# Kernel tuning notes

Hardware: AMD Instinct MI355X
Metric: run time of the kernel (lower is better)

The kernel has to match this reference:

```python
import jax, jax.numpy as jnp
import numpy as np
from jax.ops import segment_sum

N_NODES = 100000
N_EDGES = 1600000

def setup_inputs() -> dict:
    key = jax.random.key(0)
    ks = jax.random.split(key, 16)
    s = 0.1
    return {
        "x": jax.random.normal(ks[0], (N_NODES, 8), jnp.float32),
        "edge_index": jax.random.randint(ks[1], (2, N_EDGES), 0, N_NODES, jnp.int32),
        "W1l": jax.random.normal(ks[2], (8, 128)) * s,
        "W1r": jax.random.normal(ks[3], (8, 128)) * s,
        "b1": jnp.zeros((128,)),
        "W2l": jax.random.normal(ks[4], (128, 128)) * s,
        "W2r": jax.random.normal(ks[5], (128, 128)) * s,
        "b2": jnp.zeros((128,)),
        "W3l": jax.random.normal(ks[6], (128, 1)) * s,
        "W3r": jax.random.normal(ks[7], (128, 1)) * s,
        "b3": jnp.zeros((1,)),
        "Ta1_W": jax.random.normal(ks[8], (4, 8, 8)) * s,
        "Ta1_b": jnp.zeros((8,)),
        "Ta2_W": jax.random.normal(ks[9], (4, 8, 1)) * s,
        "Ta2_b": jnp.zeros((1,)),
        "Tb1_W": jax.random.normal(ks[10], (10, 8, 8)) * s,
        "Tb1_b": jnp.zeros((8,)),
        "Tb2_W": jax.random.normal(ks[11], (10, 8, 1)) * s,
        "Tb2_b": jnp.zeros((1,)),
        "lin2_W": jax.random.normal(ks[12], (2, 1)) * s,
        "lin2_b": jnp.zeros((1,)),
        "lin1_W": jax.random.normal(ks[13], (2, 1)) * s,
        "lin1_b": jnp.zeros((1,)),
    }

def reference(x, edge_index, W1l, W1r, b1, W2l, W2r, b2, W3l, W3r, b3,
              Ta1_W, Ta1_b, Ta2_W, Ta2_b, Tb1_W, Tb1_b, Tb2_W, Tb2_b,
              lin2_W, lin2_b, lin1_W, lin1_b):
    N = x.shape[0]
    src, dst = edge_index[0], edge_index[1]  # message flows src -> dst

    # in-degree of each target node (edge weight = 1)
    deg = segment_sum(jnp.ones_like(src, dtype=x.dtype), dst, num_segments=N)

    # --- SAGEConv: lin_l(mean_{j in N(i)} x_j) + lin_r(x_i) + bias ---
    inv_deg = jnp.where(deg > 0, 1.0 / jnp.maximum(deg, 1.0), 0.0)
    def sage(h, Wl, Wr, b):
        agg = segment_sum(h[src], dst, num_segments=N) * inv_deg[:, None]
        return agg @ Wl + h @ Wr + b

    # --- TAGConv: sym-normalized adjacency powers, no self loops ---
    dinv = jnp.where(deg > 0, jax.lax.rsqrt(jnp.maximum(deg, 1.0)), 0.0)
    norm = dinv[src] * dinv[dst]  # [E]
    def tag(h, Ws, b):  # Ws: [K+1, in, out]
        out = h @ Ws[0]
        for k in range(1, Ws.shape[0]):
            h = segment_sum(h[src] * norm[:, None], dst, num_segments=N)
            out = out + h @ Ws[k]
        return out + b

    relu = jax.nn.relu
    x1 = relu(sage(x, W1l, W1r, b1))
    x1 = relu(sage(x1, W2l, W2r, b2))
    x1 = relu(sage(x1, W3l, W3r, b3))

    x2 = relu(tag(x, Ta1_W, Ta1_b))
    x2 = relu(tag(x2, Ta2_W, Ta2_b))

    x3 = relu(tag(x, Tb1_W, Tb1_b))
    x3 = relu(tag(x3, Tb2_W, Tb2_b))

    x23 = relu(jnp.concatenate([x2, x3], axis=1) @ lin2_W + lin2_b)
    out = relu(jnp.concatenate([x1, x23], axis=1) @ lin1_W + lin1_b)
    return out
```

## Files before the change

### kernel.cpp

```cpp
#include <hip/hip_runtime.h>

#define NN 100000
#define NE 1600000
#define TPB 256

__global__ void k_init(int* __restrict__ deg, int* __restrict__ cursor, int* __restrict__ counter) {
    int i = blockIdx.x * TPB + threadIdx.x;
    if (i < NN) { deg[i] = 0; cursor[i] = 0; }
    if (i == 0) counter[0] = 0;
}

__global__ void k_deg(const int* __restrict__ dst, int* __restrict__ deg) {
    int e = blockIdx.x * TPB + threadIdx.x;
    if (e < NE) atomicAdd(&deg[dst[e]], 1);
}

__global__ void k_prep(const int* __restrict__ deg, float* __restrict__ inv_deg,
                       float* __restrict__ dinv, int* __restrict__ row_start,
                       int* __restrict__ counter) {
    int i = blockIdx.x * TPB + threadIdx.x;
    int lane = threadIdx.x & 63;
    int d = (i < NN) ? deg[i] : 0;
    int incl = d;
    #pragma unroll
    for (int o = 1; o < 64; o <<= 1) {
        int v = __shfl_up(incl, o, 64);
        if (lane >= o) incl += v;
    }
    int total = __shfl(incl, 63, 64);
    int base = 0;
    if (lane == 63) base = atomicAdd(counter, total);
    base = __shfl(base, 63, 64);
    if (i < NN) {
        row_start[i] = base + incl - d;
        inv_deg[i] = d > 0 ? 1.0f / (float)d : 0.0f;
        dinv[i]    = d > 0 ? 1.0f / sqrtf((float)d) : 0.0f;
    }
}

__global__ void k_fill(const int* __restrict__ src, const int* __restrict__ dst,
                       const int* __restrict__ row_start, int* __restrict__ cursor,
                       int* __restrict__ col) {
    int e = blockIdx.x * TPB + threadIdx.x;
    if (e < NE) {
        int d = dst[e];
        int p = atomicAdd(&cursor[d], 1);
        col[row_start[d] + p] = src[e];
    }
}

__global__ void k_meanprop8(const float* __restrict__ h, const int* __restrict__ row_start,
                            const int* __restrict__ deg, const float* __restrict__ inv_deg,
                            const int* __restrict__ col, float* __restrict__ out) {
    int t = blockIdx.x * TPB + threadIdx.x;
    if (t >= NN * 2) return;
    int n = t >> 1, half = t & 1;
    int rs = row_start[n], end = rs + deg[n];
    const float4* h4 = (const float4*)h;
    float4 s0 = make_float4(0,0,0,0), s1 = make_float4(0,0,0,0);
    int e = rs + half;
    for (; e + 2 < end; e += 4) {
        int c0 = col[e] * 2, c1 = col[e + 2] * 2;
        float4 a0 = h4[c0], a1 = h4[c0 + 1], b0 = h4[c1], b1 = h4[c1 + 1];
        s0.x += a0.x + b0.x; s0.y += a0.y + b0.y; s0.z += a0.z + b0.z; s0.w += a0.w + b0.w;
        s1.x += a1.x + b1.x; s1.y += a1.y + b1.y; s1.z += a1.z + b1.z; s1.w += a1.w + b1.w;
    }
    if (e < end) {
        int c0 = col[e] * 2;
        float4 a0 = h4[c0], a1 = h4[c0 + 1];
        s0.x += a0.x; s0.y += a0.y; s0.z += a0.z; s0.w += a0.w;
        s1.x += a1.x; s1.y += a1.y; s1.z += a1.z; s1.w += a1.w;
    }
    s0.x += __shfl_xor(s0.x, 1, 64); s0.y += __shfl_xor(s0.y, 1, 64);
    s0.z += __shfl_xor(s0.z, 1, 64); s0.w += __shfl_xor(s0.w, 1, 64);
    s1.x += __shfl_xor(s1.x, 1, 64); s1.y += __shfl_xor(s1.y, 1, 64);
    s1.z += __shfl_xor(s1.z, 1, 64); s1.w += __shfl_xor(s1.w, 1, 64);
    float w = inv_deg[n];
    float4 o = (half == 0) ? s0 : s1;
    o.x *= w; o.y *= w; o.z *= w; o.w *= w;
    ((float4*)out)[n * 2 + half] = o;
}

__global__ __launch_bounds__(1024) void k_meanprop128T(const float* __restrict__ h,
                              const int* __restrict__ row_start,
                              const int* __restrict__ deg, const float* __restrict__ inv_deg,
                              const int* __restrict__ col, float* __restrict__ outT) {
    __shared__ float t[128][33];
    int n0 = blockIdx.x * 32;
    int tid = threadIdx.x;
    int nl = tid >> 5;
    int f4 = tid & 31;
    int n = n0 + nl;
    int rs = row_start[n], end = rs + deg[n];
    const float4* h4 = (const float4*)h;
    float4 s = make_float4(0.f, 0.f, 0.f, 0.f);
    int e = rs;
    for (; e + 3 < end; e += 4) {
        float4 v0 = h4[(size_t)col[e] * 32 + f4];
        float4 v1 = h4[(size_t)col[e + 1] * 32 + f4];
        float4 v2 = h4[(size_t)col[e + 2] * 32 + f4];
        float4 v3 = h4[(size_t)col[e + 3] * 32 + f4];
        s.x += (v0.x + v1.x) + (v2.x + v3.x);
        s.y += (v0.y + v1.y) + (v2.y + v3.y);
        s.z += (v0.z + v1.z) + (v2.z + v3.z);
        s.w += (v0.w + v1.w) + (v2.w + v3.w);
    }
    for (; e < end; ++e) {
        float4 v = h4[(size_t)col[e] * 32 + f4];
        s.x += v.x; s.y += v.y; s.z += v.z; s.w += v.w;
    }
    float w = inv_deg[n];
    t[f4 * 4 + 0][nl] = s.x * w;
    t[f4 * 4 + 1][nl] = s.y * w;
    t[f4 * 4 + 2][nl] = s.z * w;
    t[f4 * 4 + 3][nl] = s.w * w;
    __syncthreads();
    int k = tid >> 3;
    int q = tid & 7;
    float4 v = make_float4(t[k][q * 4], t[k][q * 4 + 1], t[k][q * 4 + 2], t[k][q * 4 + 3]);
    *(float4*)(outT + (size_t)k * NN + n0 + q * 4) = v;
}

__global__ void k_tagstep(const float* __restrict__ q, const int* __restrict__ row_start,
                          const int* __restrict__ deg, const float* __restrict__ dinv,
                          const int* __restrict__ col, float* __restrict__ qout,
                          const float* __restrict__ Wa, const float* __restrict__ Wb,
                          float* __restrict__ outa, float* __restrict__ outb,
                          const float* __restrict__ ba, const float* __restrict__ bb,
                          int fina, int finb) {
    int t = blockIdx.x * TPB + threadIdx.x;
    if (t >= NN * 8) return;
    int n = t >> 3, qd = t & 7;
    int half = qd & 1, epar = qd >> 1;
    int rs = row_start[n], end = rs + deg[n];
    const float4* q4 = (const float4*)q;
    float4 s = make_float4(0,0,0,0);
    int e = rs + epar;
    for (; e + 4 < end; e += 8) {
        int c0 = col[e] * 2 + half, c1 = col[e + 4] * 2 + half;
        float4 a = q4[c0], b = q4[c1];
        s.x += a.x + b.x; s.y += a.y + b.y; s.z += a.z + b.z; s.w += a.w + b.w;
    }
    if (e < end) {
        float4 a = q4[col[e] * 2 + half];
        s.x += a.x; s.y += a.y; s.z += a.z; s.w += a.w;
    }
    #pragma unroll
    for (int o = 2; o < 8; o <<= 1) {
        s.x += __shfl_xor(s.x, o, 64); s.y += __shfl_xor(s.y, o, 64);
        s.z += __shfl_xor(s.z, o, 64); s.w += __shfl_xor(s.w, o, 64);
    }
    float dn = dinv[n];
    float m0 = s.x * dn, m1 = s.y * dn, m2 = s.z * dn, m3 = s.w * dn;
    if (qout && epar == 0) {
        ((float4*)qout)[n * 2 + half] = make_float4(m0 * dn, m1 * dn, m2 * dn, m3 * dn);
    }
    float o0 = __shfl_xor(m0, 1, 64), o1 = __shfl_xor(m1, 1, 64);
    float o2 = __shfl_xor(m2, 1, 64), o3 = __shfl_xor(m3, 1, 64);
    float h[8];
    if (half) {
        h[0] = o0; h[1] = o1; h[2] = o2; h[3] = o3;
        h[4] = m0; h[5] = m1; h[6] = m2; h[7] = m3;
    } else {
        h[0] = m0; h[1] = m1; h[2] = m2; h[3] = m3;
        h[4] = o0; h[5] = o1; h[6] = o2; h[7] = o3;
    }
    int f = qd;
    if (Wa) {
        float v = outa[(size_t)n * 8 + f];
        #pragma unroll
        for (int j = 0; j < 8; ++j) v += h[j] * Wa[j * 8 + f];
        if (fina) v = fmaxf(v + ba[f], 0.f);
        outa[(size_t)n * 8 + f] = v;
    }
    {
        float v = outb[(size_t)n * 8 + f];
        #pragma unroll
        for (int j = 0; j < 8; ++j) v += h[j] * Wb[j * 8 + f];
        if (finb) v = fmaxf(v + bb[f], 0.f);
        outb[(size_t)n * 8 + f] = v;
    }
}

__global__ void k_symprop1n(const float* __restrict__ qin, const float* __restrict__ yk,
                            const int* __restrict__ row_start, const int* __restrict__ deg,
                            const float* __restrict__ dinv, const int* __restrict__ col,
                            float* __restrict__ qout, int qstride) {
    int t = blockIdx.x * TPB + threadIdx.x;
    if (t >= NN * 8) return;
    int n = t >> 3, qd = t & 7;
    int rs = row_start[n], d = deg[n];
    float s = 0.f;
    for (int e = rs + qd; e < rs + d; e += 8) s += qin[col[e]];
    s += __shfl_xor(s, 1, 64);
    s += __shfl_xor(s, 2, 64);
    s += __shfl_xor(s, 4, 64);
    if (qd == 0) {
        float dn = dinv[n];
        qout[(size_t)n * qstride] = dn * (dn * s + yk[n]);
    }
}

__global__ void k_symprop2(const float* __restrict__ q2in, const float* __restrict__ yka,
                           const float* __restrict__ ykb, const int* __restrict__ row_start,
                           const int* __restrict__ deg, const float* __restrict__ dinv,
                           const int* __restrict__ col, float* __restrict__ q2out) {
    int t = blockIdx.x * TPB + threadIdx.x;
    if (t >= NN * 8) return;
    int n = t >> 3, qd = t & 7;
    int rs = row_start[n], d = deg[n];
    const float2* q2 = (const float2*)q2in;
    float sa = 0.f, sb = 0.f;
    for (int e = rs + qd; e < rs + d; e += 8) {
        float2 v = q2[col[e]];
        sa += v.x; sb += v.y;
    }
    sa += __shfl_xor(sa, 1, 64); sa += __shfl_xor(sa, 2, 64); sa += __shfl_xor(sa, 4, 64);
    sb += __shfl_xor(sb, 1, 64); sb += __shfl_xor(sb, 2, 64); sb += __shfl_xor(sb, 4, 64);
    if (qd == 0) {
        float dn = dinv[n];
        ((float2*)q2out)[n] = make_float2(dn * (dn * sa + yka[n]),
                                          dn * (dn * sb + ykb[n]));
    }
}

__global__ void k_symprop2fin(const float* __restrict__ q2in, const float* __restrict__ yka,
                              const float* __restrict__ ykb, const int* __restrict__ row_start,
                              const int* __restrict__ deg, const float* __restrict__ dinv,
                              const int* __restrict__ col,
                              const float* __restrict__ biasa, const float* __restrict__ biasb,
                              const float* __restrict__ x1f,
                              const float* __restrict__ l2w, const float* __restrict__ l2b,
                              const float* __restrict__ l1w, const float* __restrict__ l1b,
                              float* __restrict__ out) {
    int t = blockIdx.x * TPB + threadIdx.x;
    if (t >= NN * 8) return;
    int n = t >> 3, qd = t & 7;
    int rs = row_start[n], d = deg[n];
    const float2* q2 = (const float2*)q2in;
    float sa = 0.f, sb = 0.f;
    for (int e = rs + qd; e < rs + d; e += 8) {
        float2 v = q2[col[e]];
        sa += v.x; sb += v.y;
    }
    sa += __shfl_xor(sa, 1, 64); sa += __shfl_xor(sa, 2, 64); sa += __shfl_xor(sa, 4, 64);
    sb += __shfl_xor(sb, 1, 64); sb += __shfl_xor(sb, 2, 64); sb += __shfl_xor(sb, 4, 64);
    if (qd == 0) {
        float dn = dinv[n];
        float x2 = fmaxf(dn * sa + yka[n] + biasa[0], 0.f);
        float x3 = fmaxf(dn * sb + ykb[n] + biasb[0], 0.f);
        float x23 = fmaxf(x2 * l2w[0] + x3 * l2w[1] + l2b[0], 0.f);
        out[n] = fmaxf(x1f[n] * l1w[0] + x23 * l1w[1] + l1b[0], 0.f);
    }
}

__global__ void k_red8(const float* __restrict__ ylp, const float* __restrict__ yrp,
                       float* __restrict__ yl, float* __restrict__ yr) {
    int n = blockIdx.x * TPB + threadIdx.x;
    if (n >= NN) return;
    float sl = 0.f, sr = 0.f;
    #pragma unroll
    for (int j = 0; j < 8; ++j) {
        sl += ylp[(size_t)j * NN + n];
        sr += yrp[(size_t)j * NN + n];
    }
    yl[n] = sl;
    yr[n] = sr;
}

__global__ void k_sage3(const float* __restrict__ yl, const float* __restrict__ yr,
                        const int* __restrict__ row_start, const int* __restrict__ deg,
                        const float* __restrict__ inv_deg, const int* __restrict__ col,
                        const float* __restrict__ b3, float* __restrict__ x1f) {
    int t = blockIdx.x * TPB + threadIdx.x;
    if (t >= NN * 8) return;
    int n = t >> 3, q = t & 7;
    int rs = row_start[n], d = deg[n];
    float s = 0.f;
    for (int e = rs + q; e < rs + d; e += 8) s += yl[col[e]];
    s += __shfl_xor(s, 1, 64);
    s += __shfl_xor(s, 2, 64);
    s += __shfl_xor(s, 4, 64);
    if (q == 0) x1f[n] = fmaxf(s * inv_deg[n] + yr[n] + b3[0], 0.f);
}

__global__ __launch_bounds__(256) void k_sage1(const float* __restrict__ a8,
                        const float* __restrict__ x,
                        const float* __restrict__ W1l, const float* __restrict__ W1r,
                        const float* __restrict__ b1, float* __restrict__ x1,
                        float* __restrict__ x1T) {
    int n = blockIdx.x * 256 + threadIdx.x;
    int og = blockIdx.y * 8;
    int nc = (n < NN) ? n : (NN - 1);
    float acc[8];
    #pragma unroll
    for (int j = 0; j < 8; ++j) acc[j] = b1[og + j];
    const float* ar = a8 + (size_t)nc * 8;
    const float* xr = x + (size_t)nc * 8;
    #pragma unroll
    for (int k = 0; k < 8; ++k) {
        float av = ar[k], xv = xr[k];
        const float4* wl = (const float4*)(W1l + k * 128 + og);
        const float4* wr = (const float4*)(W1r + k * 128 + og);
        float4 l0 = wl[0], l1 = wl[1], r0 = wr[0], r1 = wr[1];
        acc[0] += av * l0.x + xv * r0.x;
        acc[1] += av * l0.y + xv * r0.y;
        acc[2] += av * l0.z + xv * r0.z;
        acc[3] += av * l0.w + xv * r0.w;
        acc[4] += av * l1.x + xv * r1.x;
        acc[5] += av * l1.y + xv * r1.y;
        acc[6] += av * l1.z + xv * r1.z;
        acc[7] += av * l1.w + xv * r1.w;
    }
    if (n < NN) {
        #pragma unroll
        for (int j = 0; j < 8; ++j) acc[j] = fmaxf(acc[j], 0.f);
        *(float4*)(x1 + (size_t)n * 128 + og)     = make_float4(acc[0], acc[1], acc[2], acc[3]);
        *(float4*)(x1 + (size_t)n * 128 + og + 4) = make_float4(acc[4], acc[5], acc[6], acc[7]);
        #pragma unroll
        for (int j = 0; j < 8; ++j)
            x1T[(size_t)(og + j) * NN + n] = acc[j];
    }
}

__global__ __launch_bounds__(256) void k_sage2f(const float* __restrict__ aT,
        const float* __restrict__ xT, const float* __restrict__ W2l,
        const float* __restrict__ W2r, const float* __restrict__ b2,
        const float* __restrict__ W3l, const float* __restrict__ W3r,
        float* __restrict__ ylp, float* __restrict__ yrp) {
    int xcd = blockIdx.x & 7;
    int s = blockIdx.x >> 3;
    int xblk = xcd * 49 + (s >> 3);
    int ogq = s & 7;
    int og = ogq * 16;
    int n0 = xblk * 256 + threadIdx.x;
    int n = (n0 < NN) ? n0 : (NN - 1);
    float acc[16];
    #pragma unroll
    for (int j = 0; j < 16; ++j) acc[j] = b2[og + j];
    const float* ap = aT + n;
    const float* xp = xT + n;
    const float* wlp = W2l + og;
    const float* wrp = W2r + og;
    #pragma unroll 4
    for (int k = 0; k < 128; ++k) {
        float a = ap[0], xv = xp[0];
        ap += NN; xp += NN;
        const float4* wl4 = (const float4*)(wlp + (k << 7));
        const float4* wr4 = (const float4*)(wrp + (k << 7));
        #pragma unroll
        for (int q = 0; q < 4; ++q) {
            float4 wl = wl4[q], wr = wr4[q];
            acc[q * 4 + 0] += a * wl.x + xv * wr.x;
            acc[q * 4 + 1] += a * wl.y + xv * wr.y;
            acc[q * 4 + 2] += a * wl.z + xv * wr.z;
            acc[q * 4 + 3] += a * wl.w + xv * wr.w;
        }
    }
    float pl = 0.f, pr = 0.f;
    #pragma unroll
    for (int j = 0; j < 16; ++j) {
        float v = fmaxf(acc[j], 0.f);
        pl += v * W3l[og + j];
        pr += v * W3r[og + j];
    }
    if (n0 < NN) {
        ylp[(size_t)ogq * NN + n0] = pl;
        yrp[(size_t)ogq * NN + n0] = pr;
    }
}

__global__ void k_taginit(const float* __restrict__ x, const float* __restrict__ TaW,
                          const float* __restrict__ TbW, const float* __restrict__ dinv,
                          float* __restrict__ outa, float* __restrict__ outb,
                          float* __restrict__ q0) {
    int t = blockIdx.x * TPB + threadIdx.x;
    if (t >= NN * 8) return;
    int n = t >> 3, o = t & 7;
    const float* xr = x + (size_t)n * 8;
    float sa = 0.f, sb = 0.f;
    #pragma unroll
    for (int j = 0; j < 8; ++j) {
        float v = xr[j];
        sa += v * TaW[j * 8 + o];
        sb += v * TbW[j * 8 + o];
    }
    outa[t] = sa;
    outb[t] = sb;
    q0[t] = xr[o] * dinv[n];
}

__global__ void k_tag2projAB(const float* __restrict__ outa, const float* __restrict__ outb,
                             const float* __restrict__ TaW2, const float* __restrict__ TbW2,
                             float* __restrict__ ya, float* __restrict__ yb,
                             const float* __restrict__ dinv,
                             float* __restrict__ q2a, float* __restrict__ qb0) {
    int n = blockIdx.x * TPB + threadIdx.x;
    if (n >= NN) return;
    float dn = dinv[n];
    float ha[8], hb[8];
    #pragma unroll
    for (int j = 0; j < 8; ++j) ha[j] = outa[(size_t)n * 8 + j];
    #pragma unroll
    for (int j = 0; j < 8; ++j) hb[j] = outb[(size_t)n * 8 + j];
    #pragma unroll
    for (int k = 0; k < 4; ++k) {
        float s = 0.f;
        #pragma unroll
        for (int j = 0; j < 8; ++j) s += ha[j] * TaW2[k * 8 + j];
        if (k == 3) q2a[(size_t)n * 2] = s * dn;
        else        ya[(size_t)k * NN + n] = s;
    }
    #pragma unroll
    for (int k = 0; k < 10; ++k) {
        float s = 0.f;
        #pragma unroll
        for (int j = 0; j < 8; ++j) s += hb[j] * TbW2[k * 8 + j];
        if (k == 9) qb0[n] = s * dn;
        else        yb[(size_t)k * NN + n] = s;
    }
}

#define GL(kern, n, ...) \
    kern<<<dim3((unsigned)(((long)(n) + TPB - 1) / TPB)), dim3(TPB), 0, stream>>>(__VA_ARGS__)

extern "C" void kernel_launch(void* const* d_in, const int* in_sizes, int n_in,
                              void* d_out, int out_size, void* d_ws, size_t ws_size,
                              hipStream_t stream) {
    (void)in_sizes; (void)n_in; (void)out_size; (void)ws_size;
    const float* x   = (const float*)d_in[0];
    const int*   ei  = (const int*)d_in[1];
    const int*   src = ei;
    const int*   dst = ei + NE;
    const float* W1l = (const float*)d_in[2];
    const float* W1r = (const float*)d_in[3];
    const float* b1  = (const float*)d_in[4];
    const float* W2l = (const float*)d_in[5];
    const float* W2r = (const float*)d_in[6];
    const float* b2  = (const float*)d_in[7];
    const float* W3l = (const float*)d_in[8];
    const float* W3r = (const float*)d_in[9];
    const float* b3  = (const float*)d_in[10];
    const float* TaW1 = (const float*)d_in[11];
    const float* TaB1 = (const float*)d_in[12];
    const float* TaW2 = (const float*)d_in[13];
    const float* TaB2 = (const float*)d_in[14];
    const float* TbW1 = (const float*)d_in[15];
    const float* TbB1 = (const float*)d_in[16];
    const float* TbW2 = (const float*)d_in[17];
    const float* TbB2 = (const float*)d_in[18];
    const float* l2w = (const float*)d_in[19];
    const float* l2b = (const float*)d_in[20];
    const float* l1w = (const float*)d_in[21];
    const float* l1b = (const float*)d_in[22];
    float* out = (float*)d_out;

    char* p = (char*)d_ws;
    size_t off = 0;
    auto alloc = [&](size_t bytes) -> void* {
        void* r = p + off;
        off = (off + bytes + 255) & ~(size_t)255;
        return r;
    };
    int*   deg       = (int*)  alloc((size_t)NN * 4);
    float* inv_deg   = (float*)alloc((size_t)NN * 4);
    float* dinv      = (float*)alloc((size_t)NN * 4);
    int*   row_start = (int*)  alloc((size_t)NN * 4);
    int*   cursor    = (int*)  alloc((size_t)NN * 4);
    int*   counter   = (int*)  alloc(256);
    int*   col       = (int*)  alloc((size_t)NE * 4);
    float* a8        = (float*)alloc((size_t)NN * 8 * 4);
    float* qA        = (float*)alloc((size_t)NN * 8 * 4);
    float* qB        = (float*)alloc((size_t)NN * 8 * 4);
    float* outa      = (float*)alloc((size_t)NN * 8 * 4);
    float* outb      = (float*)alloc((size_t)NN * 8 * 4);
    float* x1        = (float*)alloc((size_t)NN * 128 * 4);
    float* a128T     = (float*)alloc((size_t)NN * 128 * 4);
    float* x1T       = (float*)alloc((size_t)NN * 128 * 4);
    float* ylp       = (float*)alloc((size_t)NN * 8 * 4);
    float* yrp       = (float*)alloc((size_t)NN * 8 * 4);
    float* yl        = (float*)alloc((size_t)NN * 4);
    float* yr        = (float*)alloc((size_t)NN * 4);
    float* x1f       = (float*)alloc((size_t)NN * 4);
    float* tA        = (float*)alloc((size_t)NN * 4);
    float* tB        = (float*)alloc((size_t)NN * 4);
    float* qb0       = (float*)alloc((size_t)NN * 4);
    float* q2a       = (float*)alloc((size_t)NN * 8);
    float* q2b       = (float*)alloc((size_t)NN * 8);
    float* ya        = (float*)alloc((size_t)NN * 4 * 4);
    float* yb        = (float*)alloc((size_t)NN * 10 * 4);

    GL(k_init, NN, deg, cursor, counter);
    GL(k_deg, NE, dst, deg);
    GL(k_prep, NN, deg, inv_deg, dinv, row_start, counter);
    GL(k_fill, NE, src, dst, row_start, cursor, col);

    GL(k_meanprop8, (long)NN * 2, x, row_start, deg, inv_deg, col, a8);
    k_sage1<<<dim3((NN + 255) / 256, 16), dim3(256), 0, stream>>>(a8, x, W1l, W1r, b1, x1, x1T);
    k_meanprop128T<<<dim3(NN / 32), dim3(1024), 0, stream>>>(x1, row_start, deg, inv_deg, col, a128T);
    k_sage2f<<<dim3(3136), dim3(256), 0, stream>>>(a128T, x1T, W2l, W2r, b2, W3l, W3r, ylp, yrp);
    GL(k_red8, NN, ylp, yrp, yl, yr);
    GL(k_sage3, (long)NN * 8, yl, yr, row_start, deg, inv_deg, col, b3, x1f);

    GL(k_taginit, (long)NN * 8, x, TaW1, TbW1, dinv, outa, outb, qA);
    {
        float* qcur = qA;
        float* qnext = qB;
        for (int k = 1; k <= 9; ++k) {
            float* qout = (k < 9) ? qnext : nullptr;
            const float* Wa = (k <= 3) ? (TaW1 + (size_t)k * 64) : nullptr;
            GL(k_tagstep, (long)NN * 8, qcur, row_start, deg, dinv, col, qout,
               Wa, TbW1 + (size_t)k * 64, outa, outb, TaB1, TbB1,
               (k == 3) ? 1 : 0, (k == 9) ? 1 : 0);
            if (qout) { float* tmp = qcur; qcur = qnext; qnext = tmp; }
        }
    }

    GL(k_tag2projAB, NN, outa, outb, TaW2, TbW2, ya, yb, dinv, q2a, qb0);

    GL(k_symprop1n, (long)NN * 8, qb0, yb + 8 * NN, row_start, deg, dinv, col, tA, 1);
    GL(k_symprop1n, (long)NN * 8, tA,  yb + 7 * NN, row_start, deg, dinv, col, tB, 1);
    GL(k_symprop1n, (long)NN * 8, tB,  yb + 6 * NN, row_start, deg, dinv, col, tA, 1);
    GL(k_symprop1n, (long)NN * 8, tA,  yb + 5 * NN, row_start, deg, dinv, col, tB, 1);
    GL(k_symprop1n, (long)NN * 8, tB,  yb + 4 * NN, row_start, deg, dinv, col, tA, 1);
    GL(k_symprop1n, (long)NN * 8, tA,  yb + 3 * NN, row_start, deg, dinv, col, q2a + 1, 2);

    GL(k_symprop2, (long)NN * 8, q2a, ya + 2 * NN, yb + 2 * NN, row_start, deg, dinv, col, q2b);
    GL(k_symprop2, (long)NN * 8, q2b, ya + 1 * NN, yb + 1 * NN, row_start, deg, dinv, col, q2a);
    GL(k_symprop2fin, (long)NN * 8, q2a, ya + 0 * NN, yb + 0 * NN, row_start, deg, dinv, col,
       TaB2, TbB2, x1f, l2w, l2b, l1w, l1b, out);
}
```

Baseline: 734.9 us.

## Horizontally fuse independent SAGE and TAG branch kernels into combined launches

Turns the separate SAGE, TAG-a and TAG-b kernels into device functions and launches combined kernels whose block ranges dispatch to independent branch work. The TAG-a branch's second-layer propagation is split from the paired float2 propagation and co-scheduled alongside TAG-b steps and SAGE stages. The aim is to fill the GPU better on small, latency-bound graph kernels and cut the launch count. In exchange, block-range dispatch mixes heterogeneous blocks, including 1024-thread blocks shared with tagstep work, which may raise register and LDS pressure and reduce occupancy.

```diff
diff --git a/kernel.cpp b/kernel.cpp
--- a/kernel.cpp
+++ b/kernel.cpp
@@ -3,6 +3,17 @@
 #define NN 100000
 #define NE 1600000
 #define TPB 256
+
+#define NB_MP8    782
+#define NB_TAGI   3125
+#define NB_SAGE1  6272
+#define NB_TAG    3125
+#define NB_MP128T 3125
+#define NB_TAG1K  782
+#define NB_SAGE2F 3136
+#define NB_RED    391
+#define NB_PROP   3125
+#define NB_SAGE3  3125
 
 __global__ void k_init(int* __restrict__ deg, int* __restrict__ cursor, int* __restrict__ counter) {
     int i = blockIdx.x * TPB + threadIdx.x;
@@ -49,10 +60,10 @@
     }
 }
 
-__global__ void k_meanprop8(const float* __restrict__ h, const int* __restrict__ row_start,
-                            const int* __restrict__ deg, const float* __restrict__ inv_deg,
-                            const int* __restrict__ col, float* __restrict__ out) {
-    int t = blockIdx.x * TPB + threadIdx.x;
+__device__ __forceinline__ void dev_meanprop8(int t, const float* __restrict__ h,
+        const int* __restrict__ row_start, const int* __restrict__ deg,
+        const float* __restrict__ inv_deg, const int* __restrict__ col,
+        float* __restrict__ out) {
     if (t >= NN * 2) return;
     int n = t >> 1, half = t & 1;
     int rs = row_start[n], end = rs + deg[n];
@@ -81,13 +92,130 @@
     ((float4*)out)[n * 2 + half] = o;
 }
 
-__global__ __launch_bounds__(1024) void k_meanprop128T(const float* __restrict__ h,
-                              const int* __restrict__ row_start,
-                              const int* __restrict__ deg, const float* __restrict__ inv_deg,
-                              const int* __restrict__ col, float* __restrict__ outT) {
+__device__ __forceinline__ void dev_taginit(int t, const float* __restrict__ x,
+        const float* __restrict__ TaW, const float* __restrict__ TbW,
+        const float* __restrict__ dinv, float* __restrict__ outa,
+        float* __restrict__ outb, float* __restrict__ q0) {
+    if (t >= NN * 8) return;
+    int n = t >> 3, o = t & 7;
+    const float* xr = x + (size_t)n * 8;
+    float sa = 0.f, sb = 0.f;
+    #pragma unroll
+    for (int j = 0; j < 8; ++j) {
+        float v = xr[j];
+        sa += v * TaW[j * 8 + o];
+        sb += v * TbW[j * 8 + o];
+    }
+    outa[t] = sa;
+    outb[t] = sb;
+    q0[t] = xr[o] * dinv[n];
+}
+
+__device__ __forceinline__ void dev_tagstep(int t, const float* __restrict__ q,
+        const int* __restrict__ row_start, const int* __restrict__ deg,
+        const float* __restrict__ dinv, const int* __restrict__ col,
+        float* __restrict__ qout, const float* __restrict__ Wa,
+        const float* __restrict__ Wb, float* __restrict__ outa,
+        float* __restrict__ outb, const float* __restrict__ ba,
+        const float* __restrict__ bb, int fina, int finb) {
+    if (t >= NN * 8) return;
+    int n = t >> 3, qd = t & 7;
+    int half = qd & 1, epar = qd >> 1;
+    int rs = row_start[n], end = rs + deg[n];
+    const float4* q4 = (const float4*)q;
+    float4 s = make_float4(0,0,0,0);
+    int e = rs + epar;
+    for (; e + 4 < end; e += 8) {
+        int c0 = col[e] * 2 + half, c1 = col[e + 4] * 2 + half;
+        float4 a = q4[c0], b = q4[c1];
+        s.x += a.x + b.x; s.y += a.y + b.y; s.z += a.z + b.z; s.w += a.w + b.w;
+    }
+    if (e < end) {
+        float4 a = q4[col[e] * 2 + half];
+        s.x += a.x; s.y += a.y; s.z += a.z; s.w += a.w;
+    }
+    #pragma unroll
+    for (int o = 2; o < 8; o <<= 1) {
+        s.x += __shfl_xor(s.x, o, 64); s.y += __shfl_xor(s.y, o, 64);
+        s.z += __shfl_xor(s.z, o, 64); s.w += __shfl_xor(s.w, o, 64);
+    }
+    float dn = dinv[n];
+    float m0 = s.x * dn, m1 = s.y * dn, m2 = s.z * dn, m3 = s.w * dn;
+    if (qout && epar == 0) {
+        ((float4*)qout)[n * 2 + half] = make_float4(m0 * dn, m1 * dn, m2 * dn, m3 * dn);
+    }
+    float o0 = __shfl_xor(m0, 1, 64), o1 = __shfl_xor(m1, 1, 64);
+    float o2 = __shfl_xor(m2, 1, 64), o3 = __shfl_xor(m3, 1, 64);
+    float h[8];
+    if (half) {
+        h[0] = o0; h[1] = o1; h[2] = o2; h[3] = o3;
+        h[4] = m0; h[5] = m1; h[6] = m2; h[7] = m3;
+    } else {
+        h[0] = m0; h[1] = m1; h[2] = m2; h[3] = m3;
+        h[4] = o0; h[5] = o1; h[6] = o2; h[7] = o3;
+    }
+    int f = qd;
+    if (Wa) {
+        float v = outa[(size_t)n * 8 + f];
+        #pragma unroll
+        for (int j = 0; j < 8; ++j) v += h[j] * Wa[j * 8 + f];
+        if (fina) v = fmaxf(v + ba[f], 0.f);
+        outa[(size_t)n * 8 + f] = v;
+    }
+    {
+        float v = outb[(size_t)n * 8 + f];
+        #pragma unroll
+        for (int j = 0; j < 8; ++j) v += h[j] * Wb[j * 8 + f];
+        if (finb) v = fmaxf(v + bb[f], 0.f);
+        outb[(size_t)n * 8 + f] = v;
+    }
+}
+
+__device__ __forceinline__ void dev_sage1(int bid, int tid, const float* __restrict__ a8,
+        const float* __restrict__ x, const float* __restrict__ W1l,
+        const float* __restrict__ W1r, const float* __restrict__ b1,
+        float* __restrict__ x1, float* __restrict__ x1T) {
+    int bx = bid >> 4, by = bid & 15;
+    int n = bx * 256 + tid;
+    int og = by * 8;
+    int nc = (n < NN) ? n : (NN - 1);
+    float acc[8];
+    #pragma unroll
+    for (int j = 0; j < 8; ++j) acc[j] = b1[og + j];
+    const float* ar = a8 + (size_t)nc * 8;
+    const float* xr = x + (size_t)nc * 8;
+    #pragma unroll
+    for (int k = 0; k < 8; ++k) {
+        float av = ar[k], xv = xr[k];
+        const float4* wl = (const float4*)(W1l + k * 128 + og);
+        const float4* wr = (const float4*)(W1r + k * 128 + og);
+        float4 l0 = wl[0], l1 = wl[1], r0 = wr[0], r1 = wr[1];
+        acc[0] += av * l0.x + xv * r0.x;
+        acc[1] += av * l0.y + xv * r0.y;
+        acc[2] += av * l0.z + xv * r0.z;
+        acc[3] += av * l0.w + xv * r0.w;
+        acc[4] += av * l1.x + xv * r1.x;
+        acc[5] += av * l1.y + xv * r1.y;
+        acc[6] += av * l1.z + xv * r1.z;
+        acc[7] += av * l1.w + xv * r1.w;
+    }
+    if (n < NN) {
+        #pragma unroll
+        for (int j = 0; j < 8; ++j) acc[j] = fmaxf(acc[j], 0.f);
+        *(float4*)(x1 + (size_t)n * 128 + og)     = make_float4(acc[0], acc[1], acc[2], acc[3]);
+        *(float4*)(x1 + (size_t)n * 128 + og + 4) = make_float4(acc[4], acc[5], acc[6], acc[7]);
+        #pragma unroll
+        for (int j = 0; j < 8; ++j)
+            x1T[(size_t)(og + j) * NN + n] = acc[j];
+    }
+}
+
+__device__ __forceinline__ void dev_meanprop128T(int bid, int tid, const float* __restrict__ h,
+        const int* __restrict__ row_start, const int* __restrict__ deg,
+        const float* __restrict__ inv_deg, const int* __restrict__ col,
+        float* __restrict__ outT) {
     __shared__ float t[128][33];
-    int n0 = blockIdx.x * 32;
-    int tid = threadIdx.x;
+    int n0 = bid * 32;
     int nl = tid >> 5;
     int f4 = tid & 31;
     int n = n0 + nl;
@@ -121,219 +249,17 @@
     *(float4*)(outT + (size_t)k * NN + n0 + q * 4) = v;
 }
 
-__global__ void k_tagstep(const float* __restrict__ q, const int* __restrict__ row_start,
-                          const int* __restrict__ deg, const float* __restrict__ dinv,
-                          const int* __restrict__ col, float* __restrict__ qout,
-                          const float* __restrict__ Wa, const float* __restrict__ Wb,
-                          float* __restrict__ outa, float* __restrict__ outb,
-                          const float* __restrict__ ba, const float* __restrict__ bb,
-                          int fina, int finb) {
-    int t = blockIdx.x * TPB + threadIdx.x;
-    if (t >= NN * 8) return;
-    int n = t >> 3, qd = t & 7;
-    int half = qd & 1, epar = qd >> 1;
-    int rs = row_start[n], end = rs + deg[n];
-    const float4* q4 = (const float4*)q;
-    float4 s = make_float4(0,0,0,0);
-    int e = rs + epar;
-    for (; e + 4 < end; e += 8) {
-        int c0 = col[e] * 2 + half, c1 = col[e + 4] * 2 + half;
-        float4 a = q4[c0], b = q4[c1];
-        s.x += a.x + b.x; s.y += a.y + b.y; s.z += a.z + b.z; s.w += a.w + b.w;
-    }
-    if (e < end) {
-        float4 a = q4[col[e] * 2 + half];
-        s.x += a.x; s.y += a.y; s.z += a.z; s.w += a.w;
-    }
-    #pragma unroll
-    for (int o = 2; o < 8; o <<= 1) {
-        s.x += __shfl_xor(s.x, o, 64); s.y += __shfl_xor(s.y, o, 64);
-        s.z += __shfl_xor(s.z, o, 64); s.w += __shfl_xor(s.w, o, 64);
-    }
-    float dn = dinv[n];
-    float m0 = s.x * dn, m1 = s.y * dn, m2 = s.z * dn, m3 = s.w * dn;
-    if (qout && epar == 0) {
-        ((float4*)qout)[n * 2 + half] = make_float4(m0 * dn, m1 * dn, m2 * dn, m3 * dn);
-    }
-    float o0 = __shfl_xor(m0, 1, 64), o1 = __shfl_xor(m1, 1, 64);
-    float o2 = __shfl_xor(m2, 1, 64), o3 = __shfl_xor(m3, 1, 64);
-    float h[8];
-    if (half) {
-        h[0] = o0; h[1] = o1; h[2] = o2; h[3] = o3;
-        h[4] = m0; h[5] = m1; h[6] = m2; h[7] = m3;
-    } else {
-        h[0] = m0; h[1] = m1; h[2] = m2; h[3] = m3;
-        h[4] = o0; h[5] = o1; h[6] = o2; h[7] = o3;
-    }
-    int f = qd;
-    if (Wa) {
-        float v = outa[(size_t)n * 8 + f];
-        #pragma unroll
-        for (int j = 0; j < 8; ++j) v += h[j] * Wa[j * 8 + f];
-        if (fina) v = fmaxf(v + ba[f], 0.f);
-        outa[(size_t)n * 8 + f] = v;
-    }
-    {
-        float v = outb[(size_t)n * 8 + f];
-        #pragma unroll
-        for (int j = 0; j < 8; ++j) v += h[j] * Wb[j * 8 + f];
-        if (finb) v = fmaxf(v + bb[f], 0.f);
-        outb[(size_t)n * 8 + f] = v;
-    }
-}
-
-__global__ void k_symprop1n(const float* __restrict__ qin, const float* __restrict__ yk,
-                            const int* __restrict__ row_start, const int* __restrict__ deg,
-                            const float* __restrict__ dinv, const int* __restrict__ col,
-                            float* __restrict__ qout, int qstride) {
-    int t = blockIdx.x * TPB + threadIdx.x;
-    if (t >= NN * 8) return;
-    int n = t >> 3, qd = t & 7;
-    int rs = row_start[n], d = deg[n];
-    float s = 0.f;
-    for (int e = rs + qd; e < rs + d; e += 8) s += qin[col[e]];
-    s += __shfl_xor(s, 1, 64);
-    s += __shfl_xor(s, 2, 64);
-    s += __shfl_xor(s, 4, 64);
-    if (qd == 0) {
-        float dn = dinv[n];
-        qout[(size_t)n * qstride] = dn * (dn * s + yk[n]);
-    }
-}
-
-__global__ void k_symprop2(const float* __restrict__ q2in, const float* __restrict__ yka,
-                           const float* __restrict__ ykb, const int* __restrict__ row_start,
-                           const int* __restrict__ deg, const float* __restrict__ dinv,
-                           const int* __restrict__ col, float* __restrict__ q2out) {
-    int t = blockIdx.x * TPB + threadIdx.x;
-    if (t >= NN * 8) return;
-    int n = t >> 3, qd = t & 7;
-    int rs = row_start[n], d = deg[n];
-    const float2* q2 = (const float2*)q2in;
-    float sa = 0.f, sb = 0.f;
-    for (int e = rs + qd; e < rs + d; e += 8) {
-        float2 v = q2[col[e]];
-        sa += v.x; sb += v.y;
-    }
-    sa += __shfl_xor(sa, 1, 64); sa += __shfl_xor(sa, 2, 64); sa += __shfl_xor(sa, 4, 64);
-    sb += __shfl_xor(sb, 1, 64); sb += __shfl_xor(sb, 2, 64); sb += __shfl_xor(sb, 4, 64);
-    if (qd == 0) {
-        float dn = dinv[n];
-        ((float2*)q2out)[n] = make_float2(dn * (dn * sa + yka[n]),
-                                          dn * (dn * sb + ykb[n]));
-    }
-}
-
-__global__ void k_symprop2fin(const float* __restrict__ q2in, const float* __restrict__ yka,
-                              const float* __restrict__ ykb, const int* __restrict__ row_start,
-                              const int* __restrict__ deg, const float* __restrict__ dinv,
-                              const int* __restrict__ col,
-                              const float* __restrict__ biasa, const float* __restrict__ biasb,
-                              const float* __restrict__ x1f,
-                              const float* __restrict__ l2w, const float* __restrict__ l2b,
-                              const float* __restrict__ l1w, const float* __restrict__ l1b,
-                              float* __restrict__ out) {
-    int t = blockIdx.x * TPB + threadIdx.x;
-    if (t >= NN * 8) return;
-    int n = t >> 3, qd = t & 7;
-    int rs = row_start[n], d = deg[n];
-    const float2* q2 = (const float2*)q2in;
-    float sa = 0.f, sb = 0.f;
-    for (int e = rs + qd; e < rs + d; e += 8) {
-        float2 v = q2[col[e]];
-        sa += v.x; sb += v.y;
-    }
-    sa += __shfl_xor(sa, 1, 64); sa += __shfl_xor(sa, 2, 64); sa += __shfl_xor(sa, 4, 64);
-    sb += __shfl_xor(sb, 1, 64); sb += __shfl_xor(sb, 2, 64); sb += __shfl_xor(sb, 4, 64);
-    if (qd == 0) {
-        float dn = dinv[n];
-        float x2 = fmaxf(dn * sa + yka[n] + biasa[0], 0.f);
-        float x3 = fmaxf(dn * sb + ykb[n] + biasb[0], 0.f);
-        float x23 = fmaxf(x2 * l2w[0] + x3 * l2w[1] + l2b[0], 0.f);
-        out[n] = fmaxf(x1f[n] * l1w[0] + x23 * l1w[1] + l1b[0], 0.f);
-    }
-}
-
-__global__ void k_red8(const float* __restrict__ ylp, const float* __restrict__ yrp,
-                       float* __restrict__ yl, float* __restrict__ yr) {
-    int n = blockIdx.x * TPB + threadIdx.x;
-    if (n >= NN) return;
-    float sl = 0.f, sr = 0.f;
-    #pragma unroll
-    for (int j = 0; j < 8; ++j) {
-        sl += ylp[(size_t)j * NN + n];
-        sr += yrp[(size_t)j * NN + n];
-    }
-    yl[n] = sl;
-    yr[n] = sr;
-}
-
-__global__ void k_sage3(const float* __restrict__ yl, const float* __restrict__ yr,
-                        const int* __restrict__ row_start, const int* __restrict__ deg,
-                        const float* __restrict__ inv_deg, const int* __restrict__ col,
-                        const float* __restrict__ b3, float* __restrict__ x1f) {
-    int t = blockIdx.x * TPB + threadIdx.x;
-    if (t >= NN * 8) return;
-    int n = t >> 3, q = t & 7;
-    int rs = row_start[n], d = deg[n];
-    float s = 0.f;
-    for (int e = rs + q; e < rs + d; e += 8) s += yl[col[e]];
-    s += __shfl_xor(s, 1, 64);
-    s += __shfl_xor(s, 2, 64);
-    s += __shfl_xor(s, 4, 64);
-    if (q == 0) x1f[n] = fmaxf(s * inv_deg[n] + yr[n] + b3[0], 0.f);
-}
-
-__global__ __launch_bounds__(256) void k_sage1(const float* __restrict__ a8,
-                        const float* __restrict__ x,
-                        const float* __restrict__ W1l, const float* __restrict__ W1r,
-                        const float* __restrict__ b1, float* __restrict__ x1,
-                        float* __restrict__ x1T) {
-    int n = blockIdx.x * 256 + threadIdx.x;
-    int og = blockIdx.y * 8;
-    int nc = (n < NN) ? n : (NN - 1);
-    float acc[8];
-    #pragma unroll
-    for (int j = 0; j < 8; ++j) acc[j] = b1[og + j];
-    const float* ar = a8 + (size_t)nc * 8;
-    const float* xr = x + (size_t)nc * 8;
-    #pragma unroll
-    for (int k = 0; k < 8; ++k) {
-        float av = ar[k], xv = xr[k];
-        const float4* wl = (const float4*)(W1l + k * 128 + og);
-        const float4* wr = (const float4*)(W1r + k * 128 + og);
-        float4 l0 = wl[0], l1 = wl[1], r0 = wr[0], r1 = wr[1];
-        acc[0] += av * l0.x + xv * r0.x;
-        acc[1] += av * l0.y + xv * r0.y;
-        acc[2] += av * l0.z + xv * r0.z;
-        acc[3] += av * l0.w + xv * r0.w;
-        acc[4] += av * l1.x + xv * r1.x;
-        acc[5] += av * l1.y + xv * r1.y;
-        acc[6] += av * l1.z + xv * r1.z;
-        acc[7] += av * l1.w + xv * r1.w;
-    }
-    if (n < NN) {
-        #pragma unroll
-        for (int j = 0; j < 8; ++j) acc[j] = fmaxf(acc[j], 0.f);
-        *(float4*)(x1 + (size_t)n * 128 + og)     = make_float4(acc[0], acc[1], acc[2], acc[3]);
-        *(float4*)(x1 + (size_t)n * 128 + og + 4) = make_float4(acc[4], acc[5], acc[6], acc[7]);
-        #pragma unroll
-        for (int j = 0; j < 8; ++j)
-            x1T[(size_t)(og + j) * NN + n] = acc[j];
-    }
-}
-
-__global__ __launch_bounds__(256) void k_sage2f(const float* __restrict__ aT,
+__device__ __forceinline__ void dev_sage2f(int bid, int tid, const float* __restrict__ aT,
         const float* __restrict__ xT, const float* __restrict__ W2l,
         const float* __restrict__ W2r, const float* __restrict__ b2,
         const float* __restrict__ W3l, const float* __restrict__ W3r,
         float* __restrict__ ylp, float* __restrict__ yrp) {
-    int xcd = blockIdx.x & 7;
-    int s = blockIdx.x >> 3;
+    int xcd = bid & 7;
+    int s = bid >> 3;
     int xblk = xcd * 49 + (s >> 3);
     int ogq = s & 7;
     int og = ogq * 16;
-    int n0 = xblk * 256 + threadIdx.x;
+    int n0 = xblk * 256 + tid;
     int n = (n0 < NN) ? n0 : (NN - 1);
     float acc[16];
     #pragma unroll
@@ -370,54 +296,237 @@
     }
 }
 
-__global__ void k_taginit(const float* __restrict__ x, const float* __restrict__ TaW,
-                          const float* __restrict__ TbW, const float* __restrict__ dinv,
-                          float* __restrict__ outa, float* __restrict__ outb,
-                          float* __restrict__ q0) {
-    int t = blockIdx.x * TPB + threadIdx.x;
-    if (t >= NN * 8) return;
-    int n = t >> 3, o = t & 7;
-    const float* xr = x + (size_t)n * 8;
-    float sa = 0.f, sb = 0.f;
+__device__ __forceinline__ void dev_red8(int t, const float* __restrict__ ylp,
+        const float* __restrict__ yrp, float* __restrict__ yl, float* __restrict__ yr) {
+    if (t >= NN) return;
+    float sl = 0.f, sr = 0.f;
     #pragma unroll
     for (int j = 0; j < 8; ++j) {
-        float v = xr[j];
-        sa += v * TaW[j * 8 + o];
-        sb += v * TbW[j * 8 + o];
-    }
-    outa[t] = sa;
-    outb[t] = sb;
-    q0[t] = xr[o] * dinv[n];
-}
-
-__global__ void k_tag2projAB(const float* __restrict__ outa, const float* __restrict__ outb,
-                             const float* __restrict__ TaW2, const float* __restrict__ TbW2,
-                             float* __restrict__ ya, float* __restrict__ yb,
-                             const float* __restrict__ dinv,
-                             float* __restrict__ q2a, float* __restrict__ qb0) {
-    int n = blockIdx.x * TPB + threadIdx.x;
-    if (n >= NN) return;
-    float dn = dinv[n];
-    float ha[8], hb[8];
-    #pragma unroll
-    for (int j = 0; j < 8; ++j) ha[j] = outa[(size_t)n * 8 + j];
-    #pragma unroll
-    for (int j = 0; j < 8; ++j) hb[j] = outb[(size_t)n * 8 + j];
+        sl += ylp[(size_t)j * NN + t];
+        sr += yrp[(size_t)j * NN + t];
+    }
+    yl[t] = sl;
+    yr[t] = sr;
+}
+
+__device__ __forceinline__ void dev_projA(int t, const float* __restrict__ outa,
+        const float* __restrict__ TaW2, float* __restrict__ ya,
+        const float* __restrict__ dinv, float* __restrict__ qa0) {
+    if (t >= NN) return;
+    float dn = dinv[t];
+    float ha[8];
+    #pragma unroll
+    for (int j = 0; j < 8; ++j) ha[j] = outa[(size_t)t * 8 + j];
     #pragma unroll
     for (int k = 0; k < 4; ++k) {
         float s = 0.f;
         #pragma unroll
         for (int j = 0; j < 8; ++j) s += ha[j] * TaW2[k * 8 + j];
-        if (k == 3) q2a[(size_t)n * 2] = s * dn;
-        else        ya[(size_t)k * NN + n] = s;
-    }
+        if (k == 3) qa0[t] = s * dn;
+        else        ya[(size_t)k * NN + t] = s;
+    }
+}
+
+__device__ __forceinline__ void dev_sage3(int t, const float* __restrict__ yl,
+        const float* __restrict__ yr, const int* __restrict__ row_start,
+        const int* __restrict__ deg, const float* __restrict__ inv_deg,
+        const int* __restrict__ col, const float* __restrict__ b3,
+        float* __restrict__ x1f) {
+    if (t >= NN * 8) return;
+    int n = t >> 3, q = t & 7;
+    int rs = row_start[n], d = deg[n];
+    float s = 0.f;
+    for (int e = rs + q; e < rs + d; e += 8) s += yl[col[e]];
+    s += __shfl_xor(s, 1, 64);
+    s += __shfl_xor(s, 2, 64);
+    s += __shfl_xor(s, 4, 64);
+    if (q == 0) x1f[n] = fmaxf(s * inv_deg[n] + yr[n] + b3[0], 0.f);
+}
+
+__device__ __forceinline__ void dev_symprop1(int t, const float* __restrict__ qin,
+        const float* __restrict__ yk, const int* __restrict__ row_start,
+        const int* __restrict__ deg, const float* __restrict__ dinv,
+        const int* __restrict__ col, float* __restrict__ qout,
+        float* __restrict__ fout, const float* __restrict__ bias) {
+    if (t >= NN * 8) return;
+    int n = t >> 3, qd = t & 7;
+    int rs = row_start[n], d = deg[n];
+    float s = 0.f;
+    for (int e = rs + qd; e < rs + d; e += 8) s += qin[col[e]];
+    s += __shfl_xor(s, 1, 64);
+    s += __shfl_xor(s, 2, 64);
+    s += __shfl_xor(s, 4, 64);
+    if (qd == 0) {
+        float dn = dinv[n];
+        float v = dn * s + yk[n];
+        if (fout) fout[n] = fmaxf(v + bias[0], 0.f);
+        else      qout[n] = dn * v;
+    }
+}
+
+__global__ __launch_bounds__(256) void k_u1(const float* x, const int* row_start,
+        const int* deg, const float* inv_deg, const float* dinv, const int* col,
+        float* a8, const float* TaW1, const float* TbW1, float* outa, float* outb, float* qA) {
+    if (blockIdx.x < NB_MP8)
+        dev_meanprop8(blockIdx.x * 256 + threadIdx.x, x, row_start, deg, inv_deg, col, a8);
+    else
+        dev_taginit((blockIdx.x - NB_MP8) * 256 + threadIdx.x, x, TaW1, TbW1, dinv, outa, outb, qA);
+}
+
+__global__ __launch_bounds__(256) void k_u2(const float* a8, const float* x,
+        const float* W1l, const float* W1r, const float* b1, float* x1, float* x1T,
+        const float* qA, const int* row_start, const int* deg, const float* dinv,
+        const int* col, float* qB, const float* TaW1, const float* TbW1,
+        float* outa, float* outb) {
+    if (blockIdx.x < NB_SAGE1)
+        dev_sage1(blockIdx.x, threadIdx.x, a8, x, W1l, W1r, b1, x1, x1T);
+    else
+        dev_tagstep((blockIdx.x - NB_SAGE1) * 256 + threadIdx.x, qA, row_start, deg, dinv,
+                    col, qB, TaW1 + 64, TbW1 + 64, outa, outb, nullptr, nullptr, 0, 0);
+}
+
+__global__ __launch_bounds__(1024) void k_u3(const float* x1, const int* row_start,
+        const int* deg, const float* inv_deg, const float* dinv, const int* col,
+        float* a128T, const float* qB, float* qA, const float* TaW1, const float* TbW1,
+        float* outa, float* outb) {
+    if (blockIdx.x < NB_MP128T)
+        dev_meanprop128T(blockIdx.x, threadIdx.x, x1, row_start, deg, inv_deg, col, a128T);
+    else
+        dev_tagstep((blockIdx.x - NB_MP128T) * 1024 + threadIdx.x, qB, row_start, deg, dinv,
+                    col, qA, TaW1 + 2 * 64, TbW1 + 2 * 64, outa, outb, nullptr, nullptr, 0, 0);
+}
+
+__global__ __launch_bounds__(256) void k_u4(const float* a128T, const float* x1T,
+        const float* W2l, const float* W2r, const float* b2, const float* W3l,
+        const float* W3r, float* ylp, float* yrp,
+        const float* qA, const int* row_start, const int* deg, const float* dinv,
+        const int* col, float* qB, const float* TaW1, const float* TbW1,
+        float* outa, float* outb, const float* TaB1) {
+    if (blockIdx.x < NB_SAGE2F)
+        dev_sage2f(blockIdx.x, threadIdx.x, a128T, x1T, W2l, W2r, b2, W3l, W3r, ylp, yrp);
+    else
+        dev_tagstep((blockIdx.x - NB_SAGE2F) * 256 + threadIdx.x, qA, row_start, deg, dinv,
+                    col, qB, TaW1 + 3 * 64, TbW1 + 3 * 64, outa, outb, TaB1, nullptr, 1, 0);
+}
+
+__global__ __launch_bounds__(256) void k_u5(const float* ylp, const float* yrp,
+        float* yl, float* yr, const float* outa, const float* TaW2, float* ya,
+        const float* dinv, float* qa0) {
+    if (blockIdx.x < NB_RED)
+        dev_red8(blockIdx.x * 256 + threadIdx.x, ylp, yrp, yl, yr);
+    else
+        dev_projA((blockIdx.x - NB_RED) * 256 + threadIdx.x, outa, TaW2, ya, dinv, qa0);
+}
+
+__global__ __launch_bounds__(256) void k_u6(const float* yl, const float* yr,
+        const int* row_start, const int* deg, const float* inv_deg, const float* dinv,
+        const int* col, const float* b3, float* x1f,
+        const float* qB, float* qA, const float* TbW1, float* outa, float* outb) {
+    if (blockIdx.x < NB_SAGE3)
+        dev_sage3(blockIdx.x * 256 + threadIdx.x, yl, yr, row_start, deg, inv_deg, col, b3, x1f);
+    else
+        dev_tagstep((blockIdx.x - NB_SAGE3) * 256 + threadIdx.x, qB, row_start, deg, dinv,
+                    col, qA, nullptr, TbW1 + 4 * 64, outa, outb, nullptr, nullptr, 0, 0);
+}
+
+__global__ __launch_bounds__(256) void k_u7(const float* qa0, const float* ya2,
+        const int* row_start, const int* deg, const float* dinv, const int* col,
+        float* tA, const float* qA, float* qB, const float* TbW1,
+        float* outa, float* outb) {
+    if (blockIdx.x < NB_PROP)
+        dev_symprop1(blockIdx.x * 256 + threadIdx.x, qa0, ya2, row_start, deg, dinv, col,
+                     tA, nullptr, nullptr);
+    else
+        dev_tagstep((blockIdx.x - NB_PROP) * 256 + threadIdx.x, qA, row_start, deg, dinv,
+                    col, qB, nullptr, TbW1 + 5 * 64, outa, outb, nullptr, nullptr, 0, 0);
+}
+
+__global__ __launch_bounds__(256) void k_u8(const float* tA, const float* ya1,
+        const int* row_start, const int* deg, const float* dinv, const int* col,
+        float* tB, const float* qB, float* qA, const float* TbW1,
+        float* outa, float* outb) {
+    if (blockIdx.x < NB_PROP)
+        dev_symprop1(blockIdx.x * 256 + threadIdx.x, tA, ya1, row_start, deg, dinv, col,
+                     tB, nullptr, nullptr);
+    else
+        dev_tagstep((blockIdx.x - NB_PROP) * 256 + threadIdx.x, qB, row_start, deg, dinv,
+                    col, qA, nullptr, TbW1 + 6 * 64, outa, outb, nullptr, nullptr, 0, 0);
+}
+
+__global__ __launch_bounds__(256) void k_u9(const float* tB, const float* ya0,
+        const int* row_start, const int* deg, const float* dinv, const int* col,
+        float* x2s, const float* TaB2, const float* qA, float* qB, const float* TbW1,
+        float* outa, float* outb) {
+    if (blockIdx.x < NB_PROP)
+        dev_symprop1(blockIdx.x * 256 + threadIdx.x, tB, ya0, row_start, deg, dinv, col,
+                     nullptr, x2s, TaB2);
+    else
+        dev_tagstep((blockIdx.x - NB_PROP) * 256 + threadIdx.x, qA, row_start, deg, dinv,
+                    col, qB, nullptr, TbW1 + 7 * 64, outa, outb, nullptr, nullptr, 0, 0);
+}
+
+__global__ __launch_bounds__(256) void k_tag8(const float* qB, const int* row_start,
+        const int* deg, const float* dinv, const int* col, float* qA,
+        const float* TbW1, float* outa, float* outb) {
+    dev_tagstep(blockIdx.x * 256 + threadIdx.x, qB, row_start, deg, dinv, col, qA,
+                nullptr, TbW1 + 8 * 64, outa, outb, nullptr, nullptr, 0, 0);
+}
+
+__global__ __launch_bounds__(256) void k_tag9(const float* qA, const int* row_start,
+        const int* deg, const float* dinv, const int* col,
+        const float* TbW1, const float* TbB1, float* outa, float* outb) {
+    dev_tagstep(blockIdx.x * 256 + threadIdx.x, qA, row_start, deg, dinv, col, nullptr,
+                nullptr, TbW1 + 9 * 64, outa, outb, nullptr, TbB1, 0, 1);
+}
+
+__global__ __launch_bounds__(256) void k_projB(const float* __restrict__ outb,
+        const float* __restrict__ TbW2, float* __restrict__ yb,
+        const float* __restrict__ dinv, float* __restrict__ qb0) {
+    int t = blockIdx.x * 256 + threadIdx.x;
+    if (t >= NN) return;
+    float dn = dinv[t];
+    float hb[8];
+    #pragma unroll
+    for (int j = 0; j < 8; ++j) hb[j] = outb[(size_t)t * 8 + j];
     #pragma unroll
     for (int k = 0; k < 10; ++k) {
         float s = 0.f;
         #pragma unroll
         for (int j = 0; j < 8; ++j) s += hb[j] * TbW2[k * 8 + j];
-        if (k == 9) qb0[n] = s * dn;
-        else        yb[(size_t)k * NN + n] = s;
+        if (k == 9) qb0[t] = s * dn;
+        else        yb[(size_t)k * NN + t] = s;
+    }
+}
+
+__global__ __launch_bounds__(256) void k_bprop(const float* qin, const float* yk,
+        const int* row_start, const int* deg, const float* dinv, const int* col,
+        float* qout) {
+    dev_symprop1(blockIdx.x * 256 + threadIdx.x, qin, yk, row_start, deg, dinv, col,
+                 qout, nullptr, nullptr);
+}
+
+__global__ __launch_bounds__(256) void k_bpropfin(const float* __restrict__ qin,
+        const float* __restrict__ yb0, const int* __restrict__ row_start,
+        const int* __restrict__ deg, const float* __restrict__ dinv,
+        const int* __restrict__ col, const float* __restrict__ TbB2,
+        const float* __restrict__ x2s, const float* __restrict__ x1f,
+        const float* __restrict__ l2w, const float* __restrict__ l2b,
+        const float* __restrict__ l1w, const float* __restrict__ l1b,
+        float* __restrict__ out) {
+    int t = blockIdx.x * 256 + threadIdx.x;
+    if (t >= NN * 8) return;
+    int n = t >> 3, qd = t & 7;
+    int rs = row_start[n], d = deg[n];
+    float s = 0.f;
+    for (int e = rs + qd; e < rs + d; e += 8) s += qin[col[e]];
+    s += __shfl_xor(s, 1, 64);
+    s += __shfl_xor(s, 2, 64);
+    s += __shfl_xor(s, 4, 64);
+    if (qd == 0) {
+        float dn = dinv[n];
+        float x3 = fmaxf(dn * s + yb0[n] + TbB2[0], 0.f);
+        float x23 = fmaxf(x2s[n] * l2w[0] + x3 * l2w[1] + l2b[0], 0.f);
+        out[n] = fmaxf(x1f[n] * l1w[0] + x23 * l1w[1] + l1b[0], 0.f);
     }
 }
 
@@ -482,51 +591,49 @@
     float* yl        = (float*)alloc((size_t)NN * 4);
     float* yr        = (float*)alloc((size_t)NN * 4);
     float* x1f       = (float*)alloc((size_t)NN * 4);
+    float* x2s       = (float*)alloc((size_t)NN * 4);
     float* tA        = (float*)alloc((size_t)NN * 4);
     float* tB        = (float*)alloc((size_t)NN * 4);
+    float* qa0       = (float*)alloc((size_t)NN * 4);
     float* qb0       = (float*)alloc((size_t)NN * 4);
-    float* q2a       = (float*)alloc((size_t)NN * 8);
-    float* q2b       = (float*)alloc((size_t)NN * 8);
-    float* ya        = (float*)alloc((size_t)NN * 4 * 4);
-    float* yb        = (float*)alloc((size_t)NN * 10 * 4);
+    float* ya        = (float*)alloc((size_t)NN * 3 * 4);
+    float* yb        = (float*)alloc((size_t)NN * 9 * 4);
 
     GL(k_init, NN, deg, cursor, counter);
     GL(k_deg, NE, dst, deg);
     GL(k_prep, NN, deg, inv_deg, dinv, row_start, counter);
     GL(k_fill, NE, src, dst, row_start, cursor, col);
 
-    GL(k_meanprop8, (long)NN * 2, x, row_start, deg, inv_deg, col, a8);
-    k_sage1<<<dim3((NN + 255) / 256, 16), dim3(256), 0, stream>>>(a8, x, W1l, W1r, b1, x1, x1T);
-    k_meanprop128T<<<dim3(NN / 32), dim3(1024), 0, stream>>>(x1, row_start, deg, inv_deg, col, a128T);
-    k_sage2f<<<dim3(3136), dim3(256), 0, stream>>>(a128T, x1T, W2l, W2r, b2, W3l, W3r, ylp, yrp);
-    GL(k_red8, NN, ylp, yrp, yl, yr);
-    GL(k_sage3, (long)NN * 8, yl, yr, row_start, deg, inv_deg, col, b3, x1f);
-
-    GL(k_taginit, (long)NN * 8, x, TaW1, TbW1, dinv, outa, outb, qA);
-    {
-        float* qcur = qA;
-        float* qnext = qB;
-        for (int k = 1; k <= 9; ++k) {
-            float* qout = (k < 9) ? qnext : nullptr;
-            const float* Wa = (k <= 3) ? (TaW1 + (size_t)k * 64) : nullptr;
-            GL(k_tagstep, (long)NN * 8, qcur, row_start, deg, dinv, col, qout,
-               Wa, TbW1 + (size_t)k * 64, outa, outb, TaB1, TbB1,
-               (k == 3) ? 1 : 0, (k == 9) ? 1 : 0);
-            if (qout) { float* tmp = qcur; qcur = qnext; qnext = tmp; }
-        }
-    }
-
-    GL(k_tag2projAB, NN, outa, outb, TaW2, TbW2, ya, yb, dinv, q2a, qb0);
-
-    GL(k_symprop1n, (long)NN * 8, qb0, yb + 8 * NN, row_start, deg, dinv, col, tA, 1);
-    GL(k_symprop1n, (long)NN * 8, tA,  yb + 7 * NN, row_start, deg, dinv, col, tB, 1);
-    GL(k_symprop1n, (long)NN * 8, tB,  yb + 6 * NN, row_start, deg, dinv, col, tA, 1);
-    GL(k_symprop1n, (long)NN * 8, tA,  yb + 5 * NN, row_start, deg, dinv, col, tB, 1);
-    GL(k_symprop1n, (long)NN * 8, tB,  yb + 4 * NN, row_start, deg, dinv, col, tA, 1);
-    GL(k_symprop1n, (long)NN * 8, tA,  yb + 3 * NN, row_start, deg, dinv, col, q2a + 1, 2);
-
-    GL(k_symprop2, (long)NN * 8, q2a, ya + 2 * NN, yb + 2 * NN, row_start, deg, dinv, col, q2b);
-    GL(k_symprop2, (long)NN * 8, q2b, ya + 1 * NN, yb + 1 * NN, row_start, deg, dinv, col, q2a);
-    GL(k_symprop2fin, (long)NN * 8, q2a, ya + 0 * NN, yb + 0 * NN, row_start, deg, dinv, col,
-       TaB2, TbB2, x1f, l2w, l2b, l1w, l1b, out);
-}
+    k_u1<<<dim3(NB_MP8 + NB_TAGI), dim3(256), 0, stream>>>(
+        x, row_start, deg, inv_deg, dinv, col, a8, TaW1, TbW1, outa, outb, qA);
+    k_u2<<<dim3(NB_SAGE1 + NB_TAG), dim3(256), 0, stream>>>(
+        a8, x, W1l, W1r, b1, x1, x1T, qA, row_start, deg, dinv, col, qB, TaW1, TbW1, outa, outb);
+    k_u3<<<dim3(NB_MP128T + NB_TAG1K), dim3(1024), 0, stream>>>(
+        x1, row_start, deg, inv_deg, dinv, col, a128T, qB, qA, TaW1, TbW1, outa, outb);
+    k_u4<<<dim3(NB_SAGE2F + NB_TAG), dim3(256), 0, stream>>>(
+        a128T, x1T, W2l, W2r, b2, W3l, W3r, ylp, yrp,
+        qA, row_start, deg, dinv, col, qB, TaW1, TbW1, outa, outb, TaB1);
+    k_u5<<<dim3(NB_RED + NB_RED), dim3(256), 0, stream>>>(
+        ylp, yrp, yl, yr, outa, TaW2, ya, dinv, qa0);
+    k_u6<<<dim3(NB_SAGE3 + NB_TAG), dim3(256), 0, stream>>>(
+        yl, yr, row_start, deg, inv_deg, dinv, col, b3, x1f, qB, qA, TbW1, outa, outb);
+    k_u7<<<dim3(NB_PROP + NB_TAG), dim3(256), 0, stream>>>(
+        qa0, ya + 2 * NN, row_start, deg, dinv, col, tA, qA, qB, TbW1, outa, outb);
+    k_u8<<<dim3(NB_PROP + NB_TAG), dim3(256), 0, stream>>>(
+        tA, ya + 1 * NN, row_start, deg, dinv, col, tB, qB, qA, TbW1, outa, outb);
+    k_u9<<<dim3(NB_PROP + NB_TAG), dim3(256), 0, stream>>>(
+        tB, ya + 0 * NN, row_start, deg, dinv, col, x2s, TaB2, qA, qB, TbW1, outa, outb);
+    k_tag8<<<dim3(NB_TAG), dim3(256), 0, stream>>>(qB, row_start, deg, dinv, col, qA, TbW1, outa, outb);
+    k_tag9<<<dim3(NB_TAG), dim3(256), 0, stream>>>(qA, row_start, deg, dinv, col, TbW1, TbB1, outa, outb);
+    k_projB<<<dim3(NB_RED), dim3(256), 0, stream>>>(outb, TbW2, yb, dinv, qb0);
+    k_bprop<<<dim3(NB_PROP), dim3(256), 0, stream>>>(qb0, yb + 8 * NN, row_start, deg, dinv, col, tA);
+    k_bprop<<<dim3(NB_PROP), dim3(256), 0, stream>>>(tA,  yb + 7 * NN, row_start, deg, dinv, col, tB);
+    k_bprop<<<dim3(NB_PROP), dim3(256), 0, stream>>>(tB,  yb + 6 * NN, row_start, deg, dinv, col, tA);
+    k_bprop<<<dim3(NB_PROP), dim3(256), 0, stream>>>(tA,  yb + 5 * NN, row_start, deg, dinv, col, tB);
+    k_bprop<<<dim3(NB_PROP), dim3(256), 0, stream>>>(tB,  yb + 4 * NN, row_start, deg, dinv, col, tA);
+    k_bprop<<<dim3(NB_PROP), dim3(256), 0, stream>>>(tA,  yb + 3 * NN, row_start, deg, dinv, col, tB);
+    k_bprop<<<dim3(NB_PROP), dim3(256), 0, stream>>>(tB,  yb + 2 * NN, row_start, deg, dinv, col, tA);
+    k_bprop<<<dim3(NB_PROP), dim3(256), 0, stream>>>(tA,  yb + 1 * NN, row_start, deg, dinv, col, tB);
+    k_bpropfin<<<dim3(NB_PROP), dim3(256), 0, stream>>>(tB, yb + 0 * NN, row_start, deg, dinv, col,
+        TbB2, x2s, x1f, l2w, l2b, l1w, l1b, out);
+}
```

Result: slower. 1.032 ms (+40.4%).
